# Performance work log

Hardware: AMD Instinct MI355X
Metric: run time of the kernel (lower is better)

The kernel has to match this reference:

```python
import jax, jax.numpy as jnp
import numpy as np

B, C_IN, C_BOT, H = 256, 48, 8, 4096
SCALE = 1.0 / np.sqrt(8.0).astype(np.float32)


def setup_inputs() -> dict:
    key = jax.random.key(0)
    k1, k2, k3 = jax.random.split(key, 3)
    x = jax.random.normal(k1, (B, C_IN, H, 1), dtype=jnp.float32)
    # 1x1 conv weights, stored as [out_channels, in_channels]
    w_down = jax.random.normal(k2, (C_BOT, C_IN), dtype=jnp.float32) * (1.0 / np.sqrt(C_IN))
    w_up = jax.random.normal(k3, (C_IN, C_BOT), dtype=jnp.float32) * (1.0 / np.sqrt(C_BOT))
    return {"x": x, "w_down": w_down, "w_up": w_up}


def reference(x, w_down, w_up):
    # x: [B, 48, H, 1] -> [B, 48, H]
    xs = jnp.squeeze(x, axis=3)
    # fc_down applied (identically) for k, q, v: same weights, same input
    kqv = jnp.einsum('oc,bch->boh', w_down, xs)  # [B, 8, H]
    # attention matrix over channel dim: [B, 8, 8]
    am = jax.nn.softmax(jnp.einsum('bih,bjh->bij', kqv, kqv) * SCALE, axis=-1)
    z = jnp.einsum('bij,bjh->bih', am, kqv)       # [B, 8, H]
    out = jnp.einsum('co,boh->bch', w_up, z)      # [B, 48, H]
    return out[..., None]                          # [B, 48, H, 1]
```

## Files before the change

### kernel.cpp

```cpp
#include <hip/hip_runtime.h>

#define B_    256
#define CIN   48
#define CBOT  8
#define H_    4096
#define SCALE_ 0.35355339059327373f

__global__ __launch_bounds__(1024) void ultimus_kernel(
    const float* __restrict__ x,
    const float* __restrict__ w_down,
    const float* __restrict__ w_up,
    float* __restrict__ out)
{
    const int b = blockIdx.x;
    const int t = threadIdx.x;

    __shared__ float s_wdT[CIN * CBOT];
    __shared__ float s_wu [CIN * CBOT];
    __shared__ float s_red[16 * 36];
    __shared__ float s_am [CBOT * CBOT];

    if (t < CIN * CBOT) {
        const int c = t >> 3, o = t & 7;
        s_wdT[t] = w_down[o * CIN + c];
        s_wu[t]  = w_up[t];
    }
    __syncthreads();

    const float* xb = x + (size_t)b * (CIN * H_);
    const int h0 = t << 2;

    float kqv[CBOT][4];
    #pragma unroll
    for (int o = 0; o < CBOT; ++o)
        kqv[o][0] = kqv[o][1] = kqv[o][2] = kqv[o][3] = 0.0f;

    #pragma unroll 8
    for (int c = 0; c < CIN; ++c) {
        const float4 xv = *reinterpret_cast<const float4*>(xb + c * H_ + h0);
        #pragma unroll
        for (int o = 0; o < CBOT; ++o) {
            const float w = s_wdT[c * CBOT + o];
            kqv[o][0] += w * xv.x;
            kqv[o][1] += w * xv.y;
            kqv[o][2] += w * xv.z;
            kqv[o][3] += w * xv.w;
        }
    }

    float g[36];
    {
        int idx = 0;
        #pragma unroll
        for (int i = 0; i < CBOT; ++i) {
            #pragma unroll
            for (int j = i; j < CBOT; ++j, ++idx) {
                g[idx] = kqv[i][0] * kqv[j][0] + kqv[i][1] * kqv[j][1]
                       + kqv[i][2] * kqv[j][2] + kqv[i][3] * kqv[j][3];
            }
        }
    }
    #pragma unroll
    for (int k = 0; k < 36; ++k) {
        float v = g[k];
        v += __shfl_down(v, 32, 64);
        v += __shfl_down(v, 16, 64);
        v += __shfl_down(v,  8, 64);
        v += __shfl_down(v,  4, 64);
        v += __shfl_down(v,  2, 64);
        v += __shfl_down(v,  1, 64);
        g[k] = v;
    }
    const int wave = t >> 6;
    const int lane = t & 63;
    if (lane == 0) {
        #pragma unroll
        for (int k = 0; k < 36; ++k) s_red[wave * 36 + k] = g[k];
    }
    __syncthreads();

    if (t < 36) {
        float v = 0.0f;
        #pragma unroll
        for (int w = 0; w < 16; ++w) v += s_red[w * 36 + t];
        s_red[t] = v;
    }
    __syncthreads();

    if (t < 8) {
        float row[8];
        #pragma unroll
        for (int j = 0; j < 8; ++j) {
            const int i2 = t < j ? t : j;
            const int j2 = t < j ? j : t;
            const int tri = i2 * 8 - (i2 * (i2 - 1)) / 2 + (j2 - i2);
            row[j] = s_red[tri] * SCALE_;
        }
        float m = row[0];
        #pragma unroll
        for (int j = 1; j < 8; ++j) m = fmaxf(m, row[j]);
        float s = 0.0f;
        #pragma unroll
        for (int j = 0; j < 8; ++j) { row[j] = __expf(row[j] - m); s += row[j]; }
        const float inv = 1.0f / s;
        #pragma unroll
        for (int j = 0; j < 8; ++j) s_am[t * 8 + j] = row[j] * inv;
    }
    __syncthreads();

    float z[CBOT][4];
    #pragma unroll
    for (int o = 0; o < CBOT; ++o) {
        float a0 = 0.f, a1 = 0.f, a2 = 0.f, a3 = 0.f;
        #pragma unroll
        for (int j = 0; j < CBOT; ++j) {
            const float a = s_am[o * 8 + j];
            a0 += a * kqv[j][0];
            a1 += a * kqv[j][1];
            a2 += a * kqv[j][2];
            a3 += a * kqv[j][3];
        }
        z[o][0] = a0; z[o][1] = a1; z[o][2] = a2; z[o][3] = a3;
    }

    float* ob = out + (size_t)b * (CIN * H_);
    #pragma unroll 8
    for (int c = 0; c < CIN; ++c) {
        float4 r;
        r.x = r.y = r.z = r.w = 0.0f;
        #pragma unroll
        for (int o = 0; o < CBOT; ++o) {
            const float w = s_wu[c * CBOT + o];
            r.x += w * z[o][0];
            r.y += w * z[o][1];
            r.z += w * z[o][2];
            r.w += w * z[o][3];
        }
        *reinterpret_cast<float4*>(ob + c * H_ + h0) = r;
    }
}

extern "C" void kernel_launch(void* const* d_in, const int* in_sizes, int n_in,
                              void* d_out, int out_size, void* d_ws, size_t ws_size,
                              hipStream_t stream) {
    const float* x      = (const float*)d_in[0];
    const float* w_down = (const float*)d_in[1];
    const float* w_up   = (const float*)d_in[2];
    float* out          = (float*)d_out;

    hipLaunchKernelGGL(ultimus_kernel, dim3(B_), dim3(1024), 0, stream,
                       x, w_down, w_up, out);
}
```

Before: 378.3 us.

## Split each batch across two blocks with redundant Gram computation and fused output matrix

Launches two 512-thread blocks per batch element. Each block reads all of x for its batch so it can compute the full 8x8 Gram matrix independently, but writes only its own half of the output. The attention matrix is folded into w_up as a 48x8 matrix M, so the output becomes a single M·kqv product. This doubles x reads, presumably served largely from L2, in exchange for more blocks and better occupancy, and it removes the separate z stage.

```diff
diff --git a/kernel.cpp b/kernel.cpp
--- a/kernel.cpp
+++ b/kernel.cpp
@@ -6,45 +6,52 @@
 #define H_    4096
 #define SCALE_ 0.35355339059327373f
 
-__global__ __launch_bounds__(1024) void ultimus_kernel(
+#define NT    512
+#define HHALF 2048
+
+__global__ __launch_bounds__(NT, 4) void ultimus_half(
     const float* __restrict__ x,
     const float* __restrict__ w_down,
     const float* __restrict__ w_up,
     float* __restrict__ out)
 {
-    const int b = blockIdx.x;
+    const int s = blockIdx.x;
+    const int b = blockIdx.y;
     const int t = threadIdx.x;
 
     __shared__ float s_wdT[CIN * CBOT];
-    __shared__ float s_wu [CIN * CBOT];
-    __shared__ float s_red[16 * 36];
+    __shared__ float s_red[8 * 36];
     __shared__ float s_am [CBOT * CBOT];
+    __shared__ float s_M  [CIN * CBOT];
 
     if (t < CIN * CBOT) {
         const int c = t >> 3, o = t & 7;
         s_wdT[t] = w_down[o * CIN + c];
-        s_wu[t]  = w_up[t];
     }
     __syncthreads();
 
     const float* xb = x + (size_t)b * (CIN * H_);
-    const int h0 = t << 2;
+    const int hO = s * HHALF + (t << 2);
+    const int hT = (1 - s) * HHALF + (t << 2);
 
-    float kqv[CBOT][4];
+    float accO[CBOT][4], accT[CBOT][4];
     #pragma unroll
-    for (int o = 0; o < CBOT; ++o)
-        kqv[o][0] = kqv[o][1] = kqv[o][2] = kqv[o][3] = 0.0f;
+    for (int o = 0; o < CBOT; ++o) {
+        accO[o][0] = accO[o][1] = accO[o][2] = accO[o][3] = 0.0f;
+        accT[o][0] = accT[o][1] = accT[o][2] = accT[o][3] = 0.0f;
+    }
 
-    #pragma unroll 8
+    #pragma unroll 4
     for (int c = 0; c < CIN; ++c) {
-        const float4 xv = *reinterpret_cast<const float4*>(xb + c * H_ + h0);
+        const float4 xvO = *reinterpret_cast<const float4*>(xb + (size_t)c * H_ + hO);
+        const float4 xvT = *reinterpret_cast<const float4*>(xb + (size_t)c * H_ + hT);
         #pragma unroll
         for (int o = 0; o < CBOT; ++o) {
             const float w = s_wdT[c * CBOT + o];
-            kqv[o][0] += w * xv.x;
-            kqv[o][1] += w * xv.y;
-            kqv[o][2] += w * xv.z;
-            kqv[o][3] += w * xv.w;
+            accO[o][0] += w * xvO.x;  accO[o][1] += w * xvO.y;
+            accO[o][2] += w * xvO.z;  accO[o][3] += w * xvO.w;
+            accT[o][0] += w * xvT.x;  accT[o][1] += w * xvT.y;
+            accT[o][2] += w * xvT.z;  accT[o][3] += w * xvT.w;
         }
     }
 
@@ -55,8 +62,10 @@
         for (int i = 0; i < CBOT; ++i) {
             #pragma unroll
             for (int j = i; j < CBOT; ++j, ++idx) {
-                g[idx] = kqv[i][0] * kqv[j][0] + kqv[i][1] * kqv[j][1]
-                       + kqv[i][2] * kqv[j][2] + kqv[i][3] * kqv[j][3];
+                g[idx] = accO[i][0] * accO[j][0] + accO[i][1] * accO[j][1]
+                       + accO[i][2] * accO[j][2] + accO[i][3] * accO[j][3]
+                       + accT[i][0] * accT[j][0] + accT[i][1] * accT[j][1]
+                       + accT[i][2] * accT[j][2] + accT[i][3] * accT[j][3];
             }
         }
     }
@@ -78,11 +87,10 @@
         for (int k = 0; k < 36; ++k) s_red[wave * 36 + k] = g[k];
     }
     __syncthreads();
-
     if (t < 36) {
         float v = 0.0f;
         #pragma unroll
-        for (int w = 0; w < 16; ++w) v += s_red[w * 36 + t];
+        for (int w = 0; w < 8; ++w) v += s_red[w * 36 + t];
         s_red[t] = v;
     }
     __syncthreads();
@@ -99,44 +107,39 @@
         float m = row[0];
         #pragma unroll
         for (int j = 1; j < 8; ++j) m = fmaxf(m, row[j]);
-        float s = 0.0f;
+        float sum = 0.0f;
         #pragma unroll
-        for (int j = 0; j < 8; ++j) { row[j] = __expf(row[j] - m); s += row[j]; }
-        const float inv = 1.0f / s;
+        for (int j = 0; j < 8; ++j) { row[j] = __expf(row[j] - m); sum += row[j]; }
+        const float inv = 1.0f / sum;
         #pragma unroll
         for (int j = 0; j < 8; ++j) s_am[t * 8 + j] = row[j] * inv;
     }
     __syncthreads();
 
-    float z[CBOT][4];
-    #pragma unroll
-    for (int o = 0; o < CBOT; ++o) {
-        float a0 = 0.f, a1 = 0.f, a2 = 0.f, a3 = 0.f;
+    if (t < CIN * CBOT) {
+        const int c = t >> 3, j = t & 7;
+        float v = 0.0f;
         #pragma unroll
-        for (int j = 0; j < CBOT; ++j) {
-            const float a = s_am[o * 8 + j];
-            a0 += a * kqv[j][0];
-            a1 += a * kqv[j][1];
-            a2 += a * kqv[j][2];
-            a3 += a * kqv[j][3];
-        }
-        z[o][0] = a0; z[o][1] = a1; z[o][2] = a2; z[o][3] = a3;
+        for (int o = 0; o < CBOT; ++o)
+            v += w_up[c * CBOT + o] * s_am[o * CBOT + j];
+        s_M[t] = v;
     }
+    __syncthreads();
 
-    float* ob = out + (size_t)b * (CIN * H_);
+    float* ob = out + (size_t)b * (CIN * H_) + hO;
     #pragma unroll 8
     for (int c = 0; c < CIN; ++c) {
         float4 r;
         r.x = r.y = r.z = r.w = 0.0f;
         #pragma unroll
-        for (int o = 0; o < CBOT; ++o) {
-            const float w = s_wu[c * CBOT + o];
-            r.x += w * z[o][0];
-            r.y += w * z[o][1];
-            r.z += w * z[o][2];
-            r.w += w * z[o][3];
+        for (int j = 0; j < CBOT; ++j) {
+            const float mcj = s_M[c * CBOT + j];
+            r.x += mcj * accO[j][0];
+            r.y += mcj * accO[j][1];
+            r.z += mcj * accO[j][2];
+            r.w += mcj * accO[j][3];
         }
-        *reinterpret_cast<float4*>(ob + c * H_ + h0) = r;
+        *reinterpret_cast<float4*>(ob + (size_t)c * H_) = r;
     }
 }
 
@@ -148,6 +151,6 @@
     const float* w_up   = (const float*)d_in[2];
     float* out          = (float*)d_out;
 
-    hipLaunchKernelGGL(ultimus_kernel, dim3(B_), dim3(1024), 0, stream,
+    hipLaunchKernelGGL(ultimus_half, dim3(2, B_), dim3(NT), 0, stream,
                        x, w_down, w_up, out);
 }
```

Result: no change. 380.6 us (+0.6%).

## Prefetch x channels into a register ring and use nontemporal output stores

Applied to the files above, without the earlier changes.

The input load loop now keeps a 12-deep register ring of float4 channel loads, so several global loads are in flight while earlier channels are multiplied. The channel loop is fully unrolled and launch bounds ask for 4 blocks per CU. Output stores become nontemporal so the write-only result does not pollute cache. The extra live registers could push up register pressure or cause spills under the tighter launch bound.

```diff
diff --git a/kernel.cpp b/kernel.cpp
--- a/kernel.cpp
+++ b/kernel.cpp
@@ -6,7 +6,11 @@
 #define H_    4096
 #define SCALE_ 0.35355339059327373f
 
-__global__ __launch_bounds__(1024) void ultimus_kernel(
+#define NBUF  12
+
+typedef float vfloat4 __attribute__((ext_vector_type(4)));
+
+__global__ __launch_bounds__(1024, 4) void ultimus_kernel(
     const float* __restrict__ x,
     const float* __restrict__ w_down,
     const float* __restrict__ w_up,
@@ -27,24 +31,32 @@
     }
     __syncthreads();
 
-    const float* xb = x + (size_t)b * (CIN * H_);
     const int h0 = t << 2;
+    const float* xb = x + (size_t)b * (CIN * H_) + h0;
 
-    float kqv[CBOT][4];
+    vfloat4 buf[NBUF];
+    #pragma unroll
+    for (int i = 0; i < NBUF; ++i)
+        buf[i] = *reinterpret_cast<const vfloat4*>(xb + (size_t)i * H_);
+
+    float acc[CBOT][4];
     #pragma unroll
     for (int o = 0; o < CBOT; ++o)
-        kqv[o][0] = kqv[o][1] = kqv[o][2] = kqv[o][3] = 0.0f;
+        acc[o][0] = acc[o][1] = acc[o][2] = acc[o][3] = 0.0f;
 
-    #pragma unroll 8
+    #pragma unroll
     for (int c = 0; c < CIN; ++c) {
-        const float4 xv = *reinterpret_cast<const float4*>(xb + c * H_ + h0);
+        const vfloat4 xv = buf[c % NBUF];
+        if (c + NBUF < CIN)
+            buf[c % NBUF] =
+                *reinterpret_cast<const vfloat4*>(xb + (size_t)(c + NBUF) * H_);
         #pragma unroll
         for (int o = 0; o < CBOT; ++o) {
             const float w = s_wdT[c * CBOT + o];
-            kqv[o][0] += w * xv.x;
-            kqv[o][1] += w * xv.y;
-            kqv[o][2] += w * xv.z;
-            kqv[o][3] += w * xv.w;
+            acc[o][0] += w * xv.x;
+            acc[o][1] += w * xv.y;
+            acc[o][2] += w * xv.z;
+            acc[o][3] += w * xv.w;
         }
     }
 
@@ -55,8 +67,8 @@
         for (int i = 0; i < CBOT; ++i) {
             #pragma unroll
             for (int j = i; j < CBOT; ++j, ++idx) {
-                g[idx] = kqv[i][0] * kqv[j][0] + kqv[i][1] * kqv[j][1]
-                       + kqv[i][2] * kqv[j][2] + kqv[i][3] * kqv[j][3];
+                g[idx] = acc[i][0] * acc[j][0] + acc[i][1] * acc[j][1]
+                       + acc[i][2] * acc[j][2] + acc[i][3] * acc[j][3];
             }
         }
     }
@@ -115,18 +127,18 @@
         #pragma unroll
         for (int j = 0; j < CBOT; ++j) {
             const float a = s_am[o * 8 + j];
-            a0 += a * kqv[j][0];
-            a1 += a * kqv[j][1];
-            a2 += a * kqv[j][2];
-            a3 += a * kqv[j][3];
+            a0 += a * acc[j][0];
+            a1 += a * acc[j][1];
+            a2 += a * acc[j][2];
+            a3 += a * acc[j][3];
         }
         z[o][0] = a0; z[o][1] = a1; z[o][2] = a2; z[o][3] = a3;
     }
 
-    float* ob = out + (size_t)b * (CIN * H_);
+    float* ob = out + (size_t)b * (CIN * H_) + h0;
     #pragma unroll 8
     for (int c = 0; c < CIN; ++c) {
-        float4 r;
+        vfloat4 r;
         r.x = r.y = r.z = r.w = 0.0f;
         #pragma unroll
         for (int o = 0; o < CBOT; ++o) {
@@ -136,7 +148,7 @@
             r.z += w * z[o][2];
             r.w += w * z[o][3];
         }
-        *reinterpret_cast<float4*>(ob + c * H_ + h0) = r;
+        __builtin_nontemporal_store(r, reinterpret_cast<vfloat4*>(ob + (size_t)c * H_));
     }
 }
 
```

New measurement: 344.3 us. -9.0%, faster.
